# Performance work log

Measured on AMD Instinct MI355X. Metric: run time of the kernel, lower is better.

## Reference

```python
import jax, jax.numpy as jnp
import numpy as np

NSPECIES = 7
NRBF = 16
RCR, RCA, RMIN = 0.51, 0.35, 0.08
ETA_R = 1970.0   # nm^-2 (~19.7 A^-2)
ETA_A = 800.0    # nm^-2 (~8 A^-2)
ZETA = 32.0
N_SHFA, N_SHFZ = 8, 4
SUBLEN = N_SHFA * N_SHFZ
NPAIRS_SP = NSPECIES * (NSPECIES + 1) // 2  # 28
SHFR = jnp.asarray(np.linspace(RMIN, RCR, NRBF, endpoint=False), jnp.float32)
SHFA = jnp.asarray(np.linspace(RMIN, RCA, N_SHFA, endpoint=False), jnp.float32)
SHFZ = jnp.asarray(np.linspace(0.0, np.pi, N_SHFZ, endpoint=False) + np.pi / (2 * N_SHFZ), jnp.float32)

def _triu_index(ns):
    s1, s2 = np.triu_indices(ns)
    t = np.zeros((ns, ns), np.int32)
    pi = np.arange(len(s1), dtype=np.int32)
    t[s1, s2] = pi
    t[s2, s1] = pi
    return jnp.asarray(t)

TRIU = _triu_index(NSPECIES)

def _cutoff(d, rc):
    return jnp.where(d <= rc, 0.5 * (jnp.cos(d * (np.pi / rc)) + 1.0), 0.0)

def setup_inputs() -> dict:
    rng = np.random.default_rng(0)
    n_mol, M, L = 4000, 24, 0.9
    pos = rng.uniform(0.0, L, (n_mol, M, 3)).astype(np.float32)
    iu, ju = np.triu_indices(M, 1)
    rvec = pos[:, ju] - pos[:, iu]              # [n_mol, Pm, 3], r_ij = pos_j - pos_i
    dist = np.linalg.norm(rvec, axis=-1)
    keep = (dist > 0.02) & (dist < RCR)
    mol, pidx = np.nonzero(keep)
    pair_indices = np.stack([mol * M + iu[pidx], mol * M + ju[pidx]]).astype(np.int32)
    r_ij = rvec[mol, pidx].astype(np.float32)
    d_ij = dist[mol, pidx].astype(np.float32)[:, None]
    species = rng.integers(0, NSPECIES, n_mol * M).astype(np.int32)
    # pairs within angular cutoff (mirrors even_closer_indices)
    close_idx = np.nonzero(d_ij[:, 0] <= RCA)[0].astype(np.int32)
    # triple_by_molecule on the filtered pair list
    ai12 = pair_indices[:, close_idx]
    n = ai12.shape[1]
    ai1 = ai12.reshape(-1)
    order = np.argsort(ai1, kind='stable').astype(np.int64)
    sorted_ai1 = ai1[order]
    uniq, counts = np.unique(sorted_ai1, return_counts=True)
    pair_sizes = counts * (counts - 1) // 2
    central_atom_index = np.repeat(uniq, pair_sizes).astype(np.int32)
    starts = np.concatenate([[0], np.cumsum(counts)[:-1]])
    cmax = int(counts.max())
    ti, tj = np.triu_indices(cmax, 1)
    valid = tj[None, :] < counts[:, None]
    gi = (starts[:, None] + ti[None, :])[valid]
    gj = (starts[:, None] + tj[None, :])[valid]
    local12 = order[np.stack([gi, gj])]         # [2, T]
    sign12 = np.where(local12 < n, 1, -1).astype(np.int32)
    pair_index12 = (local12 % n).astype(np.int32)
    return {
        'd_ij': jnp.asarray(d_ij), 'r_ij': jnp.asarray(r_ij),
        'pair_indices': jnp.asarray(pair_indices), 'species': jnp.asarray(species),
        'close_idx': jnp.asarray(close_idx),
        'central_atom_index': jnp.asarray(central_atom_index),
        'pair_index12': jnp.asarray(pair_index12), 'sign12': jnp.asarray(sign12),
        'num_atoms': n_mol * M,
    }

def reference(d_ij, r_ij, pair_indices, species, close_idx, central_atom_index, pair_index12, sign12, num_atoms):
    d = d_ij[:, 0]                                                # [P]
    # radial symmetry functions * cosine cutoff
    rfv = 0.25 * jnp.exp(-ETA_R * (d[:, None] - SHFR) ** 2) * _cutoff(d, RCR)[:, None]  # [P,16]
    sp12 = species[pair_indices]                                  # [2,P]
    idx12 = pair_indices * NSPECIES + sp12[::-1]                  # [2,P]
    radial_aev = jnp.zeros((num_atoms * NSPECIES, NRBF), rfv.dtype)
    radial_aev = radial_aev.at[idx12[0]].add(rfv).at[idx12[1]].add(rfv)
    radial_aev = radial_aev.reshape(num_atoms, NSPECIES * NRBF)
    # angular preprocessing (gather filtered pairs into triples)
    ai12c = pair_indices[:, close_idx]
    sp12c = species[ai12c]                                        # [2,Pc]
    rijc = r_ij[close_idx]                                        # [Pc,3]
    sp12s = sp12c[:, pair_index12]                                # [2,2,T]
    rij12 = rijc[pair_index12] * sign12[..., None].astype(rijc.dtype)  # [2,T,3]
    sp12_ = jnp.where(sign12 == 1, sp12s[1], sp12s[0])            # [2,T]
    # angular symmetry functions (TorchANI-style)
    v1, v2 = rij12[0], rij12[1]
    d1 = jnp.linalg.norm(v1, axis=-1)
    d2 = jnp.linalg.norm(v2, axis=-1)
    cosang = 0.95 * jnp.sum(v1 * v2, -1) / (d1 * d2)
    ang = jnp.arccos(cosang)
    fcj = _cutoff(d1, RCA) * _cutoff(d2, RCA)
    f1 = ((1.0 + jnp.cos(ang[:, None] - SHFZ)) * 0.5) ** ZETA     # [T,4]
    f2 = jnp.exp(-ETA_A * ((d1 + d2)[:, None] * 0.5 - SHFA) ** 2) # [T,8]
    ang_terms = 2.0 * (f2[:, :, None] * f1[:, None, :]).reshape(-1, SUBLEN) * fcj[:, None]
    # scatter into per-atom, per-species-pair slots
    idx = central_atom_index * NPAIRS_SP + TRIU[sp12_[0], sp12_[1]]
    ang_aev = jnp.zeros((num_atoms * NPAIRS_SP, SUBLEN), ang_terms.dtype).at[idx].add(ang_terms)
    ang_aev = ang_aev.reshape(num_atoms, NPAIRS_SP * SUBLEN)
    return jnp.concatenate([radial_aev, ang_aev], axis=-1)        # [N, 112+896]
```

## Files before the change

kernel.cpp:

```cpp
#include <hip/hip_runtime.h>
#include <math.h>

#define NSPECIES 7
#define NRBF 16
#define NPAIRS_SP 28
#define SUBLEN 32
#define ROWLEN 1008
#define ANG_OFF 112


__global__ void radial_kernel(const float* __restrict__ d_ij,
                              const int* __restrict__ pair_indices,
                              const int* __restrict__ species,
                              float* __restrict__ out,
                              int P) {
    int tid = blockIdx.x * blockDim.x + threadIdx.x;
    int p = tid >> 4;
    int k = tid & 15;
    if (p >= P) return;

    float d = d_ij[p];
    int i = pair_indices[p];
    int j = pair_indices[P + p];
    int si = species[i];
    int sj = species[j];

    float fc = (d <= 0.51f) ? 0.5f * (cosf(d * (float)(M_PI / 0.51)) + 1.0f) : 0.0f;
    float shfr = 0.08f + (float)k * 0.026875f;
    float diff = d - shfr;
    float rfv = 0.25f * expf(-1970.0f * diff * diff) * fc;

    atomicAdd(out + (size_t)i * ROWLEN + sj * NRBF + k, rfv);
    atomicAdd(out + (size_t)j * ROWLEN + si * NRBF + k, rfv);
}

__global__ void angular_kernel(const float* __restrict__ r_ij,
                               const int* __restrict__ pair_indices,
                               const int* __restrict__ species,
                               const int* __restrict__ close_idx,
                               const int* __restrict__ central_atom_index,
                               const int* __restrict__ pair_index12,
                               const int* __restrict__ sign12,
                               float* __restrict__ out,
                               int P, int T) {
    int tid = blockIdx.x * blockDim.x + threadIdx.x;
    int t = tid >> 5;
    int lane = tid & 31;
    if (t >= T) return;

    int p1 = pair_index12[t];
    int p2 = pair_index12[T + t];
    int s1 = sign12[t];
    int s2 = sign12[T + t];
    int ca = central_atom_index[t];

    int gp1 = close_idx[p1];
    int gp2 = close_idx[p2];

    float sg1 = (float)s1, sg2 = (float)s2;
    float v1x = r_ij[gp1 * 3 + 0] * sg1;
    float v1y = r_ij[gp1 * 3 + 1] * sg1;
    float v1z = r_ij[gp1 * 3 + 2] * sg1;
    float v2x = r_ij[gp2 * 3 + 0] * sg2;
    float v2y = r_ij[gp2 * 3 + 1] * sg2;
    float v2z = r_ij[gp2 * 3 + 2] * sg2;

    int spa = species[pair_indices[(s1 == 1 ? P : 0) + gp1]];
    int spb = species[pair_indices[(s2 == 1 ? P : 0) + gp2]];

    float d1 = sqrtf(v1x * v1x + v1y * v1y + v1z * v1z);
    float d2 = sqrtf(v2x * v2x + v2y * v2y + v2z * v2z);
    float dot = v1x * v2x + v1y * v2y + v1z * v2z;

    float cosang = 0.95f * dot / (d1 * d2);
    float sinang = sqrtf(fmaxf(1.0f - cosang * cosang, 0.0f));

    float fc1 = (d1 <= 0.35f) ? 0.5f * (cosf(d1 * (float)(M_PI / 0.35)) + 1.0f) : 0.0f;
    float fc2 = (d2 <= 0.35f) ? 0.5f * (cosf(d2 * (float)(M_PI / 0.35)) + 1.0f) : 0.0f;
    float fcj = fc1 * fc2;

    int a = lane >> 2;
    int z = lane & 3;

    float shfa = 0.08f + (float)a * 0.03375f;
    float dm = (d1 + d2) * 0.5f - shfa;
    float f2 = expf(-800.0f * dm * dm);

    const float c8 = 0.92387953251f;
    const float s8 = 0.38268343236f;
    bool mid = (z == 1) | (z == 2);
    float cmag = mid ? s8 : c8;
    float smag = mid ? c8 : s8;
    float cz = (z >= 2) ? -cmag : cmag;

    float base = 0.5f * (1.0f + cosang * cz + sinang * smag);
    float x = base * base;
    x = x * x;
    x = x * x;
    x = x * x;
    x = x * x;

    float term = 2.0f * f2 * x * fcj;

    int lo = min(spa, spb), hi = max(spa, spb);
    int triu = lo * NSPECIES - (lo * (lo - 1)) / 2 + (hi - lo);

    atomicAdd(out + (size_t)ca * ROWLEN + ANG_OFF + triu * SUBLEN + lane, term);
}

extern "C" void kernel_launch(void* const* d_in, const int* in_sizes, int n_in,
                              void* d_out, int out_size, void* d_ws, size_t ws_size,
                              hipStream_t stream) {
    const float* d_ij               = (const float*)d_in[0];
    const float* r_ij               = (const float*)d_in[1];
    const int*   pair_indices       = (const int*)d_in[2];
    const int*   species            = (const int*)d_in[3];
    const int*   close_idx          = (const int*)d_in[4];
    const int*   central_atom_index = (const int*)d_in[5];
    const int*   pair_index12       = (const int*)d_in[6];
    const int*   sign12             = (const int*)d_in[7];
    float* out = (float*)d_out;

    int P = in_sizes[0];
    int T = in_sizes[5];

    hipMemsetAsync(d_out, 0, (size_t)out_size * sizeof(float), stream);

    {
        long long threads = (long long)P * 16;
        int blocks = (int)((threads + 255) / 256);
        radial_kernel<<<blocks, 256, 0, stream>>>(d_ij, pair_indices, species, out, P);
    }
    {
        long long threads = (long long)T * 32;
        int blocks = (int)((threads + 255) / 256);
        angular_kernel<<<blocks, 256, 0, stream>>>(r_ij, pair_indices, species, close_idx,
                                                   central_atom_index, pair_index12, sign12,
                                                   out, P, T);
    }
}
```

Baseline: 251.4 us.

## Bin pairs and triples per atom and accumulate AEV rows in shared memory

Replaces the global-atomic scatter with a two-phase scheme. Pairs and triples are first binned into per-atom lists in workspace. A per-atom wavefront then accumulates the radial and angular terms into an LDS row with shared atomics and writes the row to global memory once with vectorized stores, which also removes the full output memset. The lists have fixed capacities (32 neighbors, 256 triples), so any entries beyond them are silently dropped, and per-atom load imbalance can leave lanes idle.

```diff
diff --git a/kernel.cpp b/kernel.cpp
--- a/kernel.cpp
+++ b/kernel.cpp
@@ -7,105 +7,150 @@
 #define SUBLEN 32
 #define ROWLEN 1008
 #define ANG_OFF 112
+#define RAD_CAP 32
+#define ANG_CAP 256
 
 
-__global__ void radial_kernel(const float* __restrict__ d_ij,
-                              const int* __restrict__ pair_indices,
-                              const int* __restrict__ species,
-                              float* __restrict__ out,
-                              int P) {
-    int tid = blockIdx.x * blockDim.x + threadIdx.x;
-    int p = tid >> 4;
-    int k = tid & 15;
+__global__ void bin_pairs(const int* __restrict__ pair_indices,
+                          int* __restrict__ rad_cnt, int* __restrict__ rad_list,
+                          int P) {
+    int p = blockIdx.x * blockDim.x + threadIdx.x;
     if (p >= P) return;
-
-    float d = d_ij[p];
     int i = pair_indices[p];
     int j = pair_indices[P + p];
-    int si = species[i];
-    int sj = species[j];
-
-    float fc = (d <= 0.51f) ? 0.5f * (cosf(d * (float)(M_PI / 0.51)) + 1.0f) : 0.0f;
-    float shfr = 0.08f + (float)k * 0.026875f;
-    float diff = d - shfr;
-    float rfv = 0.25f * expf(-1970.0f * diff * diff) * fc;
-
-    atomicAdd(out + (size_t)i * ROWLEN + sj * NRBF + k, rfv);
-    atomicAdd(out + (size_t)j * ROWLEN + si * NRBF + k, rfv);
+    int si = atomicAdd(&rad_cnt[i], 1);
+    if (si < RAD_CAP) rad_list[i * RAD_CAP + si] = (p << 1);
+    int sj = atomicAdd(&rad_cnt[j], 1);
+    if (sj < RAD_CAP) rad_list[j * RAD_CAP + sj] = (p << 1) | 1;
 }
 
-__global__ void angular_kernel(const float* __restrict__ r_ij,
-                               const int* __restrict__ pair_indices,
-                               const int* __restrict__ species,
-                               const int* __restrict__ close_idx,
-                               const int* __restrict__ central_atom_index,
-                               const int* __restrict__ pair_index12,
-                               const int* __restrict__ sign12,
-                               float* __restrict__ out,
-                               int P, int T) {
-    int tid = blockIdx.x * blockDim.x + threadIdx.x;
-    int t = tid >> 5;
-    int lane = tid & 31;
+__global__ void bin_triples(const int* __restrict__ central_atom_index,
+                            int* __restrict__ ang_cnt, int* __restrict__ ang_list,
+                            int T) {
+    int t = blockIdx.x * blockDim.x + threadIdx.x;
     if (t >= T) return;
+    int ca = central_atom_index[t];
+    int s = atomicAdd(&ang_cnt[ca], 1);
+    if (s < ANG_CAP) ang_list[ca * ANG_CAP + s] = t;
+}
 
-    int p1 = pair_index12[t];
-    int p2 = pair_index12[T + t];
-    int s1 = sign12[t];
-    int s2 = sign12[T + t];
-    int ca = central_atom_index[t];
 
-    int gp1 = close_idx[p1];
-    int gp2 = close_idx[p2];
+__global__ __launch_bounds__(256) void aev_kernel(
+        const float* __restrict__ d_ij,
+        const float* __restrict__ r_ij,
+        const int* __restrict__ pair_indices,
+        const int* __restrict__ species,
+        const int* __restrict__ close_idx,
+        const int* __restrict__ pair_index12,
+        const int* __restrict__ sign12,
+        const int* __restrict__ rad_cnt, const int* __restrict__ rad_list,
+        const int* __restrict__ ang_cnt, const int* __restrict__ ang_list,
+        float* __restrict__ out,
+        int P, int T, int natoms) {
+    __shared__ float rows[4][ROWLEN];
 
-    float sg1 = (float)s1, sg2 = (float)s2;
-    float v1x = r_ij[gp1 * 3 + 0] * sg1;
-    float v1y = r_ij[gp1 * 3 + 1] * sg1;
-    float v1z = r_ij[gp1 * 3 + 2] * sg1;
-    float v2x = r_ij[gp2 * 3 + 0] * sg2;
-    float v2y = r_ij[gp2 * 3 + 1] * sg2;
-    float v2z = r_ij[gp2 * 3 + 2] * sg2;
+    int w = threadIdx.x >> 6;
+    int lane = threadIdx.x & 63;
+    int a = blockIdx.x * 4 + w;
+    bool live = (a < natoms);
 
-    int spa = species[pair_indices[(s1 == 1 ? P : 0) + gp1]];
-    int spb = species[pair_indices[(s2 == 1 ? P : 0) + gp2]];
+    float* row = rows[w];
+    for (int c = lane; c < ROWLEN; c += 64) row[c] = 0.0f;
+    __syncthreads();
 
-    float d1 = sqrtf(v1x * v1x + v1y * v1y + v1z * v1z);
-    float d2 = sqrtf(v2x * v2x + v2y * v2y + v2z * v2z);
-    float dot = v1x * v2x + v1y * v2y + v1z * v2z;
+    if (live) {
+        int cnt = min(rad_cnt[a], RAD_CAP);
+        int n16 = cnt * NRBF;
+        for (int idx = lane; idx < n16; idx += 64) {
+            int s = idx >> 4;
+            int k = idx & 15;
+            int code = rad_list[a * RAD_CAP + s];
+            int p = code >> 1;
+            int side = code & 1;
+            float d = d_ij[p];
+            int other = pair_indices[(side ? 0 : P) + p];
+            int sp = species[other];
+            float fc = (d <= 0.51f) ? 0.5f * (cosf(d * (float)(M_PI / 0.51)) + 1.0f) : 0.0f;
+            float shfr = 0.08f + (float)k * 0.026875f;
+            float diff = d - shfr;
+            float rfv = 0.25f * expf(-1970.0f * diff * diff) * fc;
+            atomicAdd(&row[sp * NRBF + k], rfv);
+        }
 
-    float cosang = 0.95f * dot / (d1 * d2);
-    float sinang = sqrtf(fmaxf(1.0f - cosang * cosang, 0.0f));
+        int acnt = min(ang_cnt[a], ANG_CAP);
+        int n32 = acnt * SUBLEN;
+        for (int idx = lane; idx < n32; idx += 64) {
+            int s = idx >> 5;
+            int l = idx & 31;
+            int t = ang_list[a * ANG_CAP + s];
 
-    float fc1 = (d1 <= 0.35f) ? 0.5f * (cosf(d1 * (float)(M_PI / 0.35)) + 1.0f) : 0.0f;
-    float fc2 = (d2 <= 0.35f) ? 0.5f * (cosf(d2 * (float)(M_PI / 0.35)) + 1.0f) : 0.0f;
-    float fcj = fc1 * fc2;
+            int p1 = pair_index12[t];
+            int p2 = pair_index12[T + t];
+            int s1 = sign12[t];
+            int s2 = sign12[T + t];
+            int gp1 = close_idx[p1];
+            int gp2 = close_idx[p2];
 
-    int a = lane >> 2;
-    int z = lane & 3;
+            float sg1 = (float)s1, sg2 = (float)s2;
+            float v1x = r_ij[gp1 * 3 + 0] * sg1;
+            float v1y = r_ij[gp1 * 3 + 1] * sg1;
+            float v1z = r_ij[gp1 * 3 + 2] * sg1;
+            float v2x = r_ij[gp2 * 3 + 0] * sg2;
+            float v2y = r_ij[gp2 * 3 + 1] * sg2;
+            float v2z = r_ij[gp2 * 3 + 2] * sg2;
 
-    float shfa = 0.08f + (float)a * 0.03375f;
-    float dm = (d1 + d2) * 0.5f - shfa;
-    float f2 = expf(-800.0f * dm * dm);
+            int spa = species[pair_indices[(s1 == 1 ? P : 0) + gp1]];
+            int spb = species[pair_indices[(s2 == 1 ? P : 0) + gp2]];
 
-    const float c8 = 0.92387953251f;
-    const float s8 = 0.38268343236f;
-    bool mid = (z == 1) | (z == 2);
-    float cmag = mid ? s8 : c8;
-    float smag = mid ? c8 : s8;
-    float cz = (z >= 2) ? -cmag : cmag;
+            float d1 = sqrtf(v1x * v1x + v1y * v1y + v1z * v1z);
+            float d2 = sqrtf(v2x * v2x + v2y * v2y + v2z * v2z);
+            float dot = v1x * v2x + v1y * v2y + v1z * v2z;
 
-    float base = 0.5f * (1.0f + cosang * cz + sinang * smag);
-    float x = base * base;
-    x = x * x;
-    x = x * x;
-    x = x * x;
-    x = x * x;
+            float cosang = 0.95f * dot / (d1 * d2);
+            float sinang = sqrtf(fmaxf(1.0f - cosang * cosang, 0.0f));
 
-    float term = 2.0f * f2 * x * fcj;
+            float fc1 = (d1 <= 0.35f) ? 0.5f * (cosf(d1 * (float)(M_PI / 0.35)) + 1.0f) : 0.0f;
+            float fc2 = (d2 <= 0.35f) ? 0.5f * (cosf(d2 * (float)(M_PI / 0.35)) + 1.0f) : 0.0f;
+            float fcj = fc1 * fc2;
 
-    int lo = min(spa, spb), hi = max(spa, spb);
-    int triu = lo * NSPECIES - (lo * (lo - 1)) / 2 + (hi - lo);
+            int aa = l >> 2;
+            int z = l & 3;
+            float shfa = 0.08f + (float)aa * 0.03375f;
+            float dm = (d1 + d2) * 0.5f - shfa;
+            float f2 = expf(-800.0f * dm * dm);
 
-    atomicAdd(out + (size_t)ca * ROWLEN + ANG_OFF + triu * SUBLEN + lane, term);
+            const float c8 = 0.92387953251f;
+            const float s8 = 0.38268343236f;
+            bool mid = (z == 1) | (z == 2);
+            float cmag = mid ? s8 : c8;
+            float smag = mid ? c8 : s8;
+            float cz = (z >= 2) ? -cmag : cmag;
+
+            float base = 0.5f * (1.0f + cosang * cz + sinang * smag);
+            float x = base * base;
+            x = x * x;
+            x = x * x;
+            x = x * x;
+            x = x * x;
+
+            float term = 2.0f * f2 * x * fcj;
+
+            int lo = min(spa, spb), hi = max(spa, spb);
+            int triu = lo * NSPECIES - (lo * (lo - 1)) / 2 + (hi - lo);
+
+            atomicAdd(&row[ANG_OFF + triu * SUBLEN + l], term);
+        }
+    }
+
+    __syncthreads();
+
+    if (live) {
+        float4* dst = (float4*)(out + (size_t)a * ROWLEN);
+        const float4* src = (const float4*)row;
+        for (int c = lane; c < ROWLEN / 4; c += 64) {
+            dst[c] = src[c];
+        }
+    }
 }
 
 extern "C" void kernel_launch(void* const* d_in, const int* in_sizes, int n_in,
@@ -121,21 +166,23 @@
     const int*   sign12             = (const int*)d_in[7];
     float* out = (float*)d_out;
 
-    int P = in_sizes[0];
-    int T = in_sizes[5];
+    int P      = in_sizes[0];
+    int T      = in_sizes[5];
+    int natoms = in_sizes[3];
 
-    hipMemsetAsync(d_out, 0, (size_t)out_size * sizeof(float), stream);
+    int*  rad_cnt  = (int*)d_ws;
+    int*  ang_cnt  = rad_cnt + natoms;
+    int*  rad_list = ang_cnt + natoms;
+    int*  ang_list = rad_list + (size_t)natoms * RAD_CAP;
 
-    {
-        long long threads = (long long)P * 16;
-        int blocks = (int)((threads + 255) / 256);
-        radial_kernel<<<blocks, 256, 0, stream>>>(d_ij, pair_indices, species, out, P);
-    }
-    {
-        long long threads = (long long)T * 32;
-        int blocks = (int)((threads + 255) / 256);
-        angular_kernel<<<blocks, 256, 0, stream>>>(r_ij, pair_indices, species, close_idx,
-                                                   central_atom_index, pair_index12, sign12,
-                                                   out, P, T);
-    }
+    hipMemsetAsync(rad_cnt, 0, (size_t)natoms * 2 * sizeof(int), stream);
+
+    bin_pairs<<<(P + 255) / 256, 256, 0, stream>>>(pair_indices, rad_cnt, rad_list, P);
+    bin_triples<<<(T + 255) / 256, 256, 0, stream>>>(central_atom_index, ang_cnt, ang_list, T);
+
+    int blocks = (natoms + 3) / 4;
+    aev_kernel<<<blocks, 256, 0, stream>>>(d_ij, r_ij, pair_indices, species, close_idx,
+                                           pair_index12, sign12,
+                                           rad_cnt, rad_list, ang_cnt, ang_list,
+                                           out, P, T, natoms);
 }
```

Result: slower. 369.6 us (+47.0%).

## Fuse radial and angular AEV into per-atom-block kernel with shared-memory accumulation

Applied to the files above, without the earlier changes.

Replaces the memset plus two global-atomic kernels with a single kernel. Each block owns 12 atoms and finds its pair and triple ranges by binary search over the sorted index arrays. It accumulates radial and angular terms with LDS atomics, then writes the full rows with vectorized nontemporal stores. This removes the memset and global atomic contention. It relies on pairs being sorted by first atom and grouped into molecules of 24 atoms, and it uses about 48KB of LDS per block, which limits occupancy.

```diff
diff --git a/kernel.cpp b/kernel.cpp
--- a/kernel.cpp
+++ b/kernel.cpp
@@ -7,105 +7,142 @@
 #define SUBLEN 32
 #define ROWLEN 1008
 #define ANG_OFF 112
+#define M_ATOMS 24
+#define APB 12
+#define THREADS 512
 
+typedef float v4f __attribute__((ext_vector_type(4)));
 
-__global__ void radial_kernel(const float* __restrict__ d_ij,
-                              const int* __restrict__ pair_indices,
-                              const int* __restrict__ species,
-                              float* __restrict__ out,
-                              int P) {
-    int tid = blockIdx.x * blockDim.x + threadIdx.x;
-    int p = tid >> 4;
-    int k = tid & 15;
-    if (p >= P) return;
+__global__ __launch_bounds__(THREADS) void aev_mol_kernel(
+        const float* __restrict__ d_ij,
+        const float* __restrict__ r_ij,
+        const int* __restrict__ pair_indices,
+        const int* __restrict__ species,
+        const int* __restrict__ close_idx,
+        const int* __restrict__ central_atom_index,
+        const int* __restrict__ pair_index12,
+        const int* __restrict__ sign12,
+        float* __restrict__ out,
+        int P, int T, int natoms) {
+    __shared__ float rows[APB * ROWLEN];
 
-    float d = d_ij[p];
-    int i = pair_indices[p];
-    int j = pair_indices[P + p];
-    int si = species[i];
-    int sj = species[j];
+    int tid = threadIdx.x;
+    int base = blockIdx.x * APB;
+    if (base >= natoms) return;
+    int molbase = (base / M_ATOMS) * M_ATOMS;
 
-    float fc = (d <= 0.51f) ? 0.5f * (cosf(d * (float)(M_PI / 0.51)) + 1.0f) : 0.0f;
-    float shfr = 0.08f + (float)k * 0.026875f;
-    float diff = d - shfr;
-    float rfv = 0.25f * expf(-1970.0f * diff * diff) * fc;
+    for (int c = tid; c < APB * ROWLEN; c += THREADS) rows[c] = 0.0f;
 
-    atomicAdd(out + (size_t)i * ROWLEN + sj * NRBF + k, rfv);
-    atomicAdd(out + (size_t)j * ROWLEN + si * NRBF + k, rfv);
-}
+    int p_lo, p_hi, t_lo, t_hi;
+    {
+        int lo = 0, hi = P;
+        while (lo < hi) { int mid = (lo + hi) >> 1; if (pair_indices[mid] < molbase) lo = mid + 1; else hi = mid; }
+        p_lo = lo; hi = P;
+        while (lo < hi) { int mid = (lo + hi) >> 1; if (pair_indices[mid] < molbase + M_ATOMS) lo = mid + 1; else hi = mid; }
+        p_hi = lo;
+    }
+    {
+        int lo = 0, hi = T;
+        while (lo < hi) { int mid = (lo + hi) >> 1; if (central_atom_index[mid] < base) lo = mid + 1; else hi = mid; }
+        t_lo = lo; hi = T;
+        while (lo < hi) { int mid = (lo + hi) >> 1; if (central_atom_index[mid] < base + APB) lo = mid + 1; else hi = mid; }
+        t_hi = lo;
+    }
 
-__global__ void angular_kernel(const float* __restrict__ r_ij,
-                               const int* __restrict__ pair_indices,
-                               const int* __restrict__ species,
-                               const int* __restrict__ close_idx,
-                               const int* __restrict__ central_atom_index,
-                               const int* __restrict__ pair_index12,
-                               const int* __restrict__ sign12,
-                               float* __restrict__ out,
-                               int P, int T) {
-    int tid = blockIdx.x * blockDim.x + threadIdx.x;
-    int t = tid >> 5;
-    int lane = tid & 31;
-    if (t >= T) return;
+    __syncthreads();
 
-    int p1 = pair_index12[t];
-    int p2 = pair_index12[T + t];
-    int s1 = sign12[t];
-    int s2 = sign12[T + t];
-    int ca = central_atom_index[t];
+    int npair = p_hi - p_lo;
+    for (int idx = tid; idx < npair * NRBF; idx += THREADS) {
+        int p = p_lo + (idx >> 4);
+        int k = idx & 15;
+        float d = d_ij[p];
+        int i = pair_indices[p];
+        int j = pair_indices[P + p];
+        int si = species[i];
+        int sj = species[j];
+        float fc = (d <= 0.51f) ? 0.5f * (cosf(d * (float)(M_PI / 0.51)) + 1.0f) : 0.0f;
+        float shfr = 0.08f + (float)k * 0.026875f;
+        float diff = d - shfr;
+        float rfv = 0.25f * expf(-1970.0f * diff * diff) * fc;
+        int li = i - base;
+        int lj = j - base;
+        if ((unsigned)li < APB) atomicAdd(&rows[li * ROWLEN + sj * NRBF + k], rfv);
+        if ((unsigned)lj < APB) atomicAdd(&rows[lj * ROWLEN + si * NRBF + k], rfv);
+    }
 
-    int gp1 = close_idx[p1];
-    int gp2 = close_idx[p2];
+    int ntrip = t_hi - t_lo;
+    for (int idx = tid; idx < ntrip * SUBLEN; idx += THREADS) {
+        int t = t_lo + (idx >> 5);
+        int l = idx & 31;
 
-    float sg1 = (float)s1, sg2 = (float)s2;
-    float v1x = r_ij[gp1 * 3 + 0] * sg1;
-    float v1y = r_ij[gp1 * 3 + 1] * sg1;
-    float v1z = r_ij[gp1 * 3 + 2] * sg1;
-    float v2x = r_ij[gp2 * 3 + 0] * sg2;
-    float v2y = r_ij[gp2 * 3 + 1] * sg2;
-    float v2z = r_ij[gp2 * 3 + 2] * sg2;
+        int p1 = pair_index12[t];
+        int p2 = pair_index12[T + t];
+        int s1 = sign12[t];
+        int s2 = sign12[T + t];
+        int ca = central_atom_index[t];
+        int gp1 = close_idx[p1];
+        int gp2 = close_idx[p2];
 
-    int spa = species[pair_indices[(s1 == 1 ? P : 0) + gp1]];
-    int spb = species[pair_indices[(s2 == 1 ? P : 0) + gp2]];
+        float sg1 = (float)s1, sg2 = (float)s2;
+        float v1x = r_ij[gp1 * 3 + 0] * sg1;
+        float v1y = r_ij[gp1 * 3 + 1] * sg1;
+        float v1z = r_ij[gp1 * 3 + 2] * sg1;
+        float v2x = r_ij[gp2 * 3 + 0] * sg2;
+        float v2y = r_ij[gp2 * 3 + 1] * sg2;
+        float v2z = r_ij[gp2 * 3 + 2] * sg2;
 
-    float d1 = sqrtf(v1x * v1x + v1y * v1y + v1z * v1z);
-    float d2 = sqrtf(v2x * v2x + v2y * v2y + v2z * v2z);
-    float dot = v1x * v2x + v1y * v2y + v1z * v2z;
+        int spa = species[pair_indices[(s1 == 1 ? P : 0) + gp1]];
+        int spb = species[pair_indices[(s2 == 1 ? P : 0) + gp2]];
 
-    float cosang = 0.95f * dot / (d1 * d2);
-    float sinang = sqrtf(fmaxf(1.0f - cosang * cosang, 0.0f));
+        float d1 = sqrtf(v1x * v1x + v1y * v1y + v1z * v1z);
+        float d2 = sqrtf(v2x * v2x + v2y * v2y + v2z * v2z);
+        float dot = v1x * v2x + v1y * v2y + v1z * v2z;
 
-    float fc1 = (d1 <= 0.35f) ? 0.5f * (cosf(d1 * (float)(M_PI / 0.35)) + 1.0f) : 0.0f;
-    float fc2 = (d2 <= 0.35f) ? 0.5f * (cosf(d2 * (float)(M_PI / 0.35)) + 1.0f) : 0.0f;
-    float fcj = fc1 * fc2;
+        float cosang = 0.95f * dot / (d1 * d2);
+        float sinang = sqrtf(fmaxf(1.0f - cosang * cosang, 0.0f));
 
-    int a = lane >> 2;
-    int z = lane & 3;
+        float fc1 = (d1 <= 0.35f) ? 0.5f * (cosf(d1 * (float)(M_PI / 0.35)) + 1.0f) : 0.0f;
+        float fc2 = (d2 <= 0.35f) ? 0.5f * (cosf(d2 * (float)(M_PI / 0.35)) + 1.0f) : 0.0f;
+        float fcj = fc1 * fc2;
 
-    float shfa = 0.08f + (float)a * 0.03375f;
-    float dm = (d1 + d2) * 0.5f - shfa;
-    float f2 = expf(-800.0f * dm * dm);
+        int aa = l >> 2;
+        int z = l & 3;
+        float shfa = 0.08f + (float)aa * 0.03375f;
+        float dm = (d1 + d2) * 0.5f - shfa;
+        float f2 = expf(-800.0f * dm * dm);
 
-    const float c8 = 0.92387953251f;
-    const float s8 = 0.38268343236f;
-    bool mid = (z == 1) | (z == 2);
-    float cmag = mid ? s8 : c8;
-    float smag = mid ? c8 : s8;
-    float cz = (z >= 2) ? -cmag : cmag;
+        const float c8 = 0.92387953251f;
+        const float s8 = 0.38268343236f;
+        bool mid = (z == 1) | (z == 2);
+        float cmag = mid ? s8 : c8;
+        float smag = mid ? c8 : s8;
+        float cz = (z >= 2) ? -cmag : cmag;
 
-    float base = 0.5f * (1.0f + cosang * cz + sinang * smag);
-    float x = base * base;
-    x = x * x;
-    x = x * x;
-    x = x * x;
-    x = x * x;
+        float bse = 0.5f * (1.0f + cosang * cz + sinang * smag);
+        float x = bse * bse;
+        x = x * x;
+        x = x * x;
+        x = x * x;
+        x = x * x;
 
-    float term = 2.0f * f2 * x * fcj;
+        float term = 2.0f * f2 * x * fcj;
 
-    int lo = min(spa, spb), hi = max(spa, spb);
-    int triu = lo * NSPECIES - (lo * (lo - 1)) / 2 + (hi - lo);
+        int lo = min(spa, spb), hi = max(spa, spb);
+        int triu = lo * NSPECIES - (lo * (lo - 1)) / 2 + (hi - lo);
 
-    atomicAdd(out + (size_t)ca * ROWLEN + ANG_OFF + triu * SUBLEN + lane, term);
+        atomicAdd(&rows[(ca - base) * ROWLEN + ANG_OFF + triu * SUBLEN + l], term);
+    }
+
+    __syncthreads();
+
+    int nrows = min(APB, natoms - base);
+    v4f* dst = (v4f*)(out + (size_t)base * ROWLEN);
+    const v4f* src = (const v4f*)rows;
+    int n4 = nrows * (ROWLEN / 4);
+    for (int c = tid; c < n4; c += THREADS) {
+        v4f v = src[c];
+        __builtin_nontemporal_store(v, &dst[c]);
+    }
 }
 
 extern "C" void kernel_launch(void* const* d_in, const int* in_sizes, int n_in,
@@ -121,21 +158,13 @@
     const int*   sign12             = (const int*)d_in[7];
     float* out = (float*)d_out;
 
-    int P = in_sizes[0];
-    int T = in_sizes[5];
+    int P      = in_sizes[0];
+    int T      = in_sizes[5];
+    int natoms = in_sizes[3];
 
-    hipMemsetAsync(d_out, 0, (size_t)out_size * sizeof(float), stream);
-
-    {
-        long long threads = (long long)P * 16;
-        int blocks = (int)((threads + 255) / 256);
-        radial_kernel<<<blocks, 256, 0, stream>>>(d_ij, pair_indices, species, out, P);
-    }
-    {
-        long long threads = (long long)T * 32;
-        int blocks = (int)((threads + 255) / 256);
-        angular_kernel<<<blocks, 256, 0, stream>>>(r_ij, pair_indices, species, close_idx,
-                                                   central_atom_index, pair_index12, sign12,
-                                                   out, P, T);
-    }
+    int blocks = (natoms + APB - 1) / APB;
+    aev_mol_kernel<<<blocks, THREADS, 0, stream>>>(d_ij, r_ij, pair_indices, species,
+                                                   close_idx, central_atom_index,
+                                                   pair_index12, sign12,
+                                                   out, P, T, natoms);
 }
```

Result: slower. 306.1 us (+21.7%).
